# Kernel tuning notes

Hardware: AMD Instinct MI355X
Metric: run time of the kernel (lower is better)

## Reference

```python
import jax, jax.numpy as jnp
import numpy as np

B, T, H, L = 32, 256, 1024, 2
FORGET_BIAS = 1.0


def setup_inputs() -> dict:
    key = jax.random.key(0)
    k1, k2, k3, k4 = jax.random.split(key, 4)
    x = jax.random.normal(k1, (B, T, H), dtype=jnp.float32)
    lengths = jax.random.randint(k2, (B,), 1, T + 1, dtype=jnp.int32)
    Wx = jax.random.normal(k3, (L, H, 4 * H), dtype=jnp.float32) * 0.02
    Wh = jax.random.normal(k4, (L, H, 4 * H), dtype=jnp.float32) * 0.02
    b = jnp.zeros((L, 4 * H), dtype=jnp.float32)
    return {"x": x, "lengths": lengths, "Wx": Wx, "Wh": Wh, "b": b}


def _lstm_layer(x, lengths, Wx, Wh, b):
    """One TF-style LSTM layer over time with dynamic_rnn length masking.
    Gate order (i, j, f, o), forget_bias added to f. Returns (outputs, (h_T, c_T))."""
    Bb, Tt, _ = x.shape
    Hh = Wh.shape[0]
    # precompute input projections for all steps: [B, T, 4H]
    xproj = jnp.einsum('bti,ig->btg', x, Wx) + b

    def step(carry, inp):
        h, c = carry
        xt, t = inp  # xt: [B, 4H], t: scalar step index
        z = xt + h @ Wh  # [B, 4H]
        i, j, f, o = jnp.split(z, 4, axis=-1)
        c_new = jax.nn.sigmoid(f + FORGET_BIAS) * c + jax.nn.sigmoid(i) * jnp.tanh(j)
        h_new = jax.nn.sigmoid(o) * jnp.tanh(c_new)
        mask = (t < lengths)[:, None]  # [B,1]
        h2 = jnp.where(mask, h_new, h)
        c2 = jnp.where(mask, c_new, c)
        out = jnp.where(mask, h_new, 0.0)  # dynamic_rnn zeros outputs past length
        return (h2, c2), out

    init = (jnp.zeros((Bb, Hh), x.dtype), jnp.zeros((Bb, Hh), x.dtype))
    (hT, cT), outs = jax.lax.scan(step, init, (xproj.transpose(1, 0, 2), jnp.arange(Tt)))
    return outs.transpose(1, 0, 2), (hT, cT)


def reference(x, lengths, Wx, Wh, b):
    inp = x
    hs, cs = [], []
    for l in range(L):  # fixed small layer stack
        inp, (hT, cT) = _lstm_layer(inp, lengths, Wx[l], Wh[l], b[l])
        hs.append(hT)
        cs.append(cT)
    # rnnout: [B,T,H]; hidden: per-layer final (c,h) like TF LSTMStateTuple
    return inp, jnp.stack(cs), jnp.stack(hs)
```

## Files before the change

### kernel.cpp

```cpp
#include <hip/hip_runtime.h>

typedef unsigned short u16;
typedef unsigned int u32;
typedef unsigned long long u64;
typedef __attribute__((ext_vector_type(8))) short short8;
typedef __attribute__((ext_vector_type(4))) float f32x4;
typedef __attribute__((ext_vector_type(4))) u32 u32x4;
typedef __attribute__((ext_vector_type(2))) u32 u32x2;

#define RN_ 8388608
#define MFMA16(a, b, c) __builtin_amdgcn_mfma_f32_16x16x32_bf16(a, b, c, 0, 0, 0)

__device__ __forceinline__ u16 f2bf(float f) {
  union { float f; u32 u; } v; v.f = f;
  u32 r = v.u + 0x7fffu + ((v.u >> 16) & 1u);
  return (u16)(r >> 16);
}
__device__ __forceinline__ float bf2f(u16 h) {
  union { u32 u; float f; } v; v.u = ((u32)h) << 16;
  return v.f;
}
__device__ __forceinline__ u32 pk2(float a, float b) {
  return (u32)f2bf(a) | ((u32)f2bf(b) << 16);
}
__device__ __forceinline__ int permcol(int R) {
  return (R & 3) * 1024 + ((R >> 5) << 3) + ((R >> 2) & 7);
}
__device__ __forceinline__ float sigm(float x) { return 1.f / (1.f + __expf(-x)); }
__device__ __forceinline__ float tanh_(float x) {
  float e = __expf(2.f * x);
  return 1.f - 2.f / (e + 1.f);
}

__global__ __launch_bounds__(256) void transpose_convert(
    const float* __restrict__ Wx, const float* __restrict__ Wh,
    u16* __restrict__ WxT1, u16* __restrict__ WxT2,
    u16* __restrict__ WhT1, u16* __restrict__ WhT2) {
  __shared__ float lds[64][65];
  const int bid = blockIdx.x, tid = threadIdx.x;
  const int sel = bid >> 10;
  const int tile = bid & 1023;
  const int kt = tile & 15, rt = tile >> 4;
  const float* src;
  u16* dst;
  if (sel == 0)      { src = Wx;                       dst = WxT1; }
  else if (sel == 1) { src = Wx + (size_t)1024 * 4096; dst = WxT2; }
  else if (sel == 2) { src = Wh;                       dst = WhT1; }
  else               { src = Wh + (size_t)1024 * 4096; dst = WhT2; }
#pragma unroll
  for (int ii = 0; ii < 16; ++ii) {
    int idx = ii * 256 + tid;
    int r = idx >> 6, c = idx & 63;
    int run = c >> 3, u = c & 7;
    int blkLoc = run >> 2, gate = run & 3;
    int g = gate * 1024 + (rt * 2 + blkLoc) * 8 + u;
    lds[r][blkLoc * 32 + u * 4 + gate] = src[(size_t)(kt * 64 + r) * 4096 + g];
  }
  __syncthreads();
#pragma unroll
  for (int ii = 0; ii < 16; ++ii) {
    int idx = ii * 256 + tid;
    int rw = idx >> 6, cw = idx & 63;
    dst[(size_t)(rt * 64 + rw) * 1024 + kt * 64 + cw] = f2bf(lds[cw][rw]);
  }
}

template <int IS2>
__device__ void gemm_grp(char* smem, int gb,
    const float* __restrict__ Af32, const u16* __restrict__ Ahp,
    const u16* __restrict__ Bt, const float* __restrict__ bias,
    u16* __restrict__ Cring, const int* flags, int* gdone) {
  u16* As = (u16*)smem;
  u16* Bs = (u16*)(smem + 16384);
  const int tid = threadIdx.x;
  const int lane = tid & 63, w = tid >> 6;
  const int wm = w >> 1, wn = w & 1;
  const int l15 = lane & 15, lq = lane >> 4;
  const int srow = tid >> 2, qd = tid & 3;
  const u32 rsw = (u32)((l15 & 7) << 4);

  for (int c = 0; c < 16; ++c) {
    if (w == 0) {
      const int thrA = IS2 ? 16 * (c + 1) : 16 * c - 48;
      const int thrB = 16 * c - 48;
      while (1) {
        bool ok = true;
        if (lane < 16) {
          u32x4 fv;
          const u32x4* fp = (const u32x4*)flags + lane;
          asm volatile("global_load_dwordx4 %0, %1, off sc0 sc1"
                       : "=v"(fv) : "v"(fp) : "memory");
          asm volatile("s_waitcnt vmcnt(0)" ::: "memory");
          ok = (int)fv[0] >= thrA && (int)fv[1] >= thrA &&
               (int)fv[2] >= thrA && (int)fv[3] >= thrA;
        } else if (IS2 && lane < 32) {
          u32x4 fv;
          const u32x4* fp = (const u32x4*)(flags + 64) + (lane - 16);
          asm volatile("global_load_dwordx4 %0, %1, off sc0 sc1"
                       : "=v"(fv) : "v"(fp) : "memory");
          asm volatile("s_waitcnt vmcnt(0)" ::: "memory");
          ok = (int)fv[0] >= thrB && (int)fv[1] >= thrB &&
               (int)fv[2] >= thrB && (int)fv[3] >= thrB;
        }
        if (__all(ok)) break;
        __builtin_amdgcn_s_sleep(8);
      }
    }
    __syncthreads();

    for (int e = 0; e < 2; ++e) {
      const int ti = gb * 2 + e;
      const int mg = ti >> 5, ng = ti & 31;

      f32x4 acc[4][4];
#pragma unroll
      for (int i = 0; i < 4; ++i)
#pragma unroll
        for (int j = 0; j < 4; ++j) acc[i][j] = (f32x4){0.f, 0.f, 0.f, 0.f};

      for (int kt = 0; kt < 16; ++kt) {
        u32x4 aw[2][2], bv[2][2];
#pragma unroll
        for (int rr = 0; rr < 2; ++rr) {
          int row = rr * 64 + srow;
          const u32x4* bp = (const u32x4*)(Bt + (size_t)(ng * 128 + row) * 1024 + kt * 64 + qd * 16);
          bv[rr][0] = bp[0]; bv[rr][1] = bp[1];
          int rg = 512 * c + mg * 128 + row;
          if (IS2) {
            int tq = rg >> 5, b2 = rg & 31;
            int p = kt * 8 + qd * 2;
            const char* ap = (const char*)Ahp + (size_t)tq * 65536 +
                             (size_t)(p * 32 + b2) * 16;
            asm volatile("global_load_dwordx4 %0, %1, off sc0 sc1"
                         : "=v"(aw[rr][0]) : "v"(ap) : "memory");
            asm volatile("global_load_dwordx4 %0, %1, off sc0 sc1"
                         : "=v"(aw[rr][1]) : "v"(ap + 512) : "memory");
          } else {
            const f32x4* ap = (const f32x4*)(Af32 +
                ((size_t)(rg & 31) * 256 + (rg >> 5)) * 1024 + kt * 64 + qd * 16);
            f32x4 a0 = ap[0], a1 = ap[1], a2 = ap[2], a3 = ap[3];
            aw[rr][0][0] = pk2(a0[0], a0[1]); aw[rr][0][1] = pk2(a0[2], a0[3]);
            aw[rr][0][2] = pk2(a1[0], a1[1]); aw[rr][0][3] = pk2(a1[2], a1[3]);
            aw[rr][1][0] = pk2(a2[0], a2[1]); aw[rr][1][1] = pk2(a2[2], a2[3]);
            aw[rr][1][2] = pk2(a3[0], a3[1]); aw[rr][1][3] = pk2(a3[2], a3[3]);
          }
        }
        __syncthreads();
        if (IS2) {
          asm volatile("s_waitcnt vmcnt(0)" ::: "memory");
          __builtin_amdgcn_sched_barrier(0);
        }
#pragma unroll
        for (int rr = 0; rr < 2; ++rr) {
          int row = rr * 64 + srow;
          u32 sw = (u32)((row & 7) << 4);
          int base = row * 128 + qd * 32;
          *(u32x4*)((char*)As + ((base) ^ sw)) = aw[rr][0];
          *(u32x4*)((char*)As + ((base + 16) ^ sw)) = aw[rr][1];
          *(u32x4*)((char*)Bs + ((base) ^ sw)) = bv[rr][0];
          *(u32x4*)((char*)Bs + ((base + 16) ^ sw)) = bv[rr][1];
        }
        __syncthreads();
#pragma unroll
        for (int k2 = 0; k2 < 2; ++k2) {
          short8 af[4], bf[4];
#pragma unroll
          for (int f = 0; f < 4; ++f) {
            af[f] = *(const short8*)((const char*)As +
                     (((wm * 64 + f * 16 + l15) * 128 + k2 * 64 + lq * 16) ^ rsw));
            bf[f] = *(const short8*)((const char*)Bs +
                     (((wn * 64 + f * 16 + l15) * 128 + k2 * 64 + lq * 16) ^ rsw));
          }
#pragma unroll
          for (int fi = 0; fi < 4; ++fi)
#pragma unroll
            for (int fj = 0; fj < 4; ++fj)
              acc[fi][fj] = MFMA16(af[fi], bf[fj], acc[fi][fj]);
        }
      }
#pragma unroll
      for (int fj = 0; fj < 4; ++fj) {
        int gc = ng * 128 + wn * 64 + fj * 16 + l15;
        float bvv = bias[permcol(gc)];
#pragma unroll
        for (int fi = 0; fi < 4; ++fi) {
          int rr0 = (c & 3) * 512 + mg * 128 + wm * 64 + fi * 16 + lq * 4;
#pragma unroll
          for (int r = 0; r < 4; ++r) {
            u32 vv = (u32)f2bf(acc[fi][fj][r] + bvv);
            const u16* cp = Cring + (size_t)(rr0 + r) * 4096 + gc;
            asm volatile("global_store_short %0, %1, off sc0 sc1"
                         :: "v"(cp), "v"(vv) : "memory");
          }
        }
      }
      __syncthreads();
    }
    asm volatile("s_waitcnt vmcnt(0)" ::: "memory");
    if (tid == 0)
      __hip_atomic_fetch_add(gdone + c, 1, __ATOMIC_RELAXED, __HIP_MEMORY_SCOPE_AGENT);
  }
}

template <int L>
__device__ void scan_grp(char* smem, int nb,
    const u16* __restrict__ xpring, const u16* __restrict__ Wt,
    const int* __restrict__ lengths, u64* hpub,
    int* flags_self, const int* gdone,
    float* __restrict__ outp, float* __restrict__ csf, float* __restrict__ hsf) {
  f32x4* partv = (f32x4*)smem;
  u16* h_stage = (u16*)(smem + 32768);
  float* out_stage = (float*)(smem + 33792);
  const int tid = threadIdx.x;
  const int lane = tid & 63, w = tid >> 6;
  const int l15 = lane & 15, q = lane >> 4;
  const int b = (w & 1) * 16 + l15;
  const int u0 = (w >> 1) * 4 + q;
  const int len = lengths[b];

  short8 afr[4][8];
#pragma unroll
  for (int tt = 0; tt < 4; ++tt)
#pragma unroll
    for (int ks = 0; ks < 8; ++ks)
      afr[tt][ks] = *(const short8*)(Wt + (size_t)(nb * 64 + tt * 16 + l15) * 1024 +
                                     w * 256 + ks * 32 + q * 8);

  f32x4 acc[4][2];
#pragma unroll
  for (int tt = 0; tt < 4; ++tt)
#pragma unroll
    for (int bc = 0; bc < 2; ++bc) acc[tt][bc] = (f32x4){0.f, 0.f, 0.f, 0.f};
  float c0 = 0.f, h0 = 0.f, c1 = 0.f, h1 = 0.f;

  for (int t = 0; t < 256; ++t) {
    if (w == 0) {
      const int cidx = t >> 4;
      while (1) {
        bool ok = true;
        if (lane < 16) {
          u32x4 fv;
          const u32x4* fp = (const u32x4*)flags_self + lane;
          asm volatile("global_load_dwordx4 %0, %1, off sc0 sc1"
                       : "=v"(fv) : "v"(fp) : "memory");
          asm volatile("s_waitcnt vmcnt(0)" ::: "memory");
          ok = (int)fv[0] >= t && (int)fv[1] >= t && (int)fv[2] >= t && (int)fv[3] >= t;
        } else if (lane == 16) {
          u32 cd;
          const int* gp = gdone + cidx;
          asm volatile("global_load_dword %0, %1, off sc0 sc1"
                       : "=v"(cd) : "v"(gp) : "memory");
          asm volatile("s_waitcnt vmcnt(0)" ::: "memory");
          ok = (int)cd >= 64;
        }
        if (__all(ok)) break;
        __builtin_amdgcn_s_sleep(1);
      }
    }
    __syncthreads();

    const u16* xa = xpring + ((size_t)((t >> 4) & 3) * 512 + (t & 15) * 32 + b) * 4096 +
                    nb * 64 + u0 * 4;
    u32x2 xpv0, xpv1;
    asm volatile("global_load_dwordx2 %0, %1, off sc0 sc1"
                 : "=v"(xpv0) : "v"(xa) : "memory");
    asm volatile("global_load_dwordx2 %0, %1, off sc0 sc1"
                 : "=v"(xpv1) : "v"(xa + 32) : "memory");

    if (t > 0) {
      const char* hp = (const char*)hpub + (size_t)(t - 1) * 65536;
      short8 bfv[16];
#pragma unroll
      for (int i = 0; i < 16; ++i) {
        const int ks = i >> 1, bc = i & 1;
        const char* p = hp + (((w * 32 + ks * 4 + q) * 32 + bc * 16 + l15) << 4);
        asm volatile("global_load_dwordx4 %0, %1, off sc0 sc1"
                     : "=v"(bfv[i]) : "v"(p) : "memory");
      }
      asm volatile("s_waitcnt vmcnt(0)" ::: "memory");
      __builtin_amdgcn_sched_barrier(0);
#pragma unroll
      for (int i = 0; i < 16; ++i) {
        const int ks = i >> 1, bc = i & 1;
        acc[0][bc] = MFMA16(afr[0][ks], bfv[i], acc[0][bc]);
        acc[1][bc] = MFMA16(afr[1][ks], bfv[i], acc[1][bc]);
        acc[2][bc] = MFMA16(afr[2][ks], bfv[i], acc[2][bc]);
        acc[3][bc] = MFMA16(afr[3][ks], bfv[i], acc[3][bc]);
      }
    } else {
      asm volatile("s_waitcnt vmcnt(0)" ::: "memory");
      __builtin_amdgcn_sched_barrier(0);
    }

#pragma unroll
    for (int tt = 0; tt < 4; ++tt)
#pragma unroll
      for (int bc = 0; bc < 2; ++bc) {
        partv[(w * 8 + tt * 2 + bc) * 64 + lane] = acc[tt][bc];
        acc[tt][bc] = (f32x4){0.f, 0.f, 0.f, 0.f};
      }
    __syncthreads();
    f32x4 s0 = (f32x4){0.f, 0.f, 0.f, 0.f};
    f32x4 s1 = (f32x4){0.f, 0.f, 0.f, 0.f};
#pragma unroll
    for (int w2 = 0; w2 < 4; ++w2) {
      s0 += partv[(w2 * 8 + w) * 64 + lane];
      s1 += partv[(w2 * 8 + 4 + w) * 64 + lane];
    }

    bool mk = t < len;
    {
      float zi = s0[0] + bf2f((u16)(xpv0[0] & 0xffffu));
      float zj = s0[1] + bf2f((u16)(xpv0[0] >> 16));
      float zf = s0[2] + bf2f((u16)(xpv0[1] & 0xffffu)) + 1.f;
      float zo = s0[3] + bf2f((u16)(xpv0[1] >> 16));
      float cn = sigm(zf) * c0 + sigm(zi) * tanh_(zj);
      float hn = sigm(zo) * tanh_(cn);
      c0 = mk ? cn : c0;
      h0 = mk ? hn : h0;
      float ov = mk ? hn : 0.f;
      h_stage[b * 16 + u0] = f2bf(ov);
      if (L) out_stage[b * 16 + u0] = ov;
    }
    {
      float zi = s1[0] + bf2f((u16)(xpv1[0] & 0xffffu));
      float zj = s1[1] + bf2f((u16)(xpv1[0] >> 16));
      float zf = s1[2] + bf2f((u16)(xpv1[1] & 0xffffu)) + 1.f;
      float zo = s1[3] + bf2f((u16)(xpv1[1] >> 16));
      float cn = sigm(zf) * c1 + sigm(zi) * tanh_(zj);
      float hn = sigm(zo) * tanh_(cn);
      c1 = mk ? cn : c1;
      h1 = mk ? hn : h1;
      float ov = mk ? hn : 0.f;
      h_stage[b * 16 + u0 + 8] = f2bf(ov);
      if (L) out_stage[b * 16 + u0 + 8] = ov;
    }
    __syncthreads();

    if (tid < 64) {
      int p = tid >> 5, bb = tid & 31;
      const u64* hsrc = (const u64*)h_stage;
      u64 v0 = hsrc[bb * 4 + p * 2], v1 = hsrc[bb * 4 + p * 2 + 1];
      u64* hd = hpub + (size_t)t * 8192 + ((size_t)((nb * 2 + p) * 32 + bb)) * 2;
      __hip_atomic_store(hd, v0, __ATOMIC_RELAXED, __HIP_MEMORY_SCOPE_AGENT);
      __hip_atomic_store(hd + 1, v1, __ATOMIC_RELAXED, __HIP_MEMORY_SCOPE_AGENT);
    }
    asm volatile("s_waitcnt vmcnt(0)" ::: "memory");
    if (tid == 0)
      __hip_atomic_store(flags_self + nb, t + 1, __ATOMIC_RELAXED,
                         __HIP_MEMORY_SCOPE_AGENT);
    if (L && tid < 128) {
      int bb = tid >> 2, part = tid & 3;
      f32x4 ov = *(const f32x4*)(out_stage + bb * 16 + part * 4);
      *(f32x4*)(outp + ((size_t)bb * 256 + t) * 1024 + nb * 16 + part * 4) = ov;
    }
  }
  csf[L * 32768 + b * 1024 + nb * 16 + u0] = c0;
  csf[L * 32768 + b * 1024 + nb * 16 + u0 + 8] = c1;
  hsf[L * 32768 + b * 1024 + nb * 16 + u0] = h0;
  hsf[L * 32768 + b * 1024 + nb * 16 + u0 + 8] = h1;
}

__global__ __launch_bounds__(256, 1) void lstm_pipe(
    const float* __restrict__ x, const int* __restrict__ lengths,
    const float* __restrict__ bias,
    const u16* __restrict__ WxT1, const u16* __restrict__ WxT2,
    const u16* __restrict__ WhT1, const u16* __restrict__ WhT2,
    u16* xp1ring, u16* xp2ring,
    u64* hpub1, u64* hpub2, int* flags, float* outp) {
  __shared__ __align__(16) char smem[35840];
  int* g1done = flags + 128;
  int* g2done = flags + 144;
  const int bid = blockIdx.x;
  float* csf = outp + RN_;
  float* hsf = csf + 65536;
  if (bid < 64)
    gemm_grp<0>(smem, bid, x, nullptr, WxT1, bias, xp1ring, flags, g1done);
  else if (bid < 128)
    scan_grp<0>(smem, bid - 64, xp1ring, WhT1, lengths, hpub1, flags, g1done,
                outp, csf, hsf);
  else if (bid < 192)
    gemm_grp<1>(smem, bid - 128, nullptr, (const u16*)hpub1, WxT2, bias + 4096,
                xp2ring, flags, g2done);
  else
    scan_grp<1>(smem, bid - 192, xp2ring, WhT2, lengths, hpub2, flags + 64, g2done,
                outp, csf, hsf);
}

#define WS_WXT1 0u
#define WS_WXT2 (8u << 20)
#define WS_WHT1 (16u << 20)
#define WS_WHT2 (24u << 20)
#define WS_XP1 (32u << 20)
#define WS_XP2 (48u << 20)
#define WS_HPUB1 (64u << 20)
#define WS_HPUB2 (80u << 20)
#define WS_FLAGS (96u << 20)

extern "C" void kernel_launch(void* const* d_in, const int* in_sizes, int n_in,
                              void* d_out, int out_size, void* d_ws, size_t ws_size,
                              hipStream_t stream) {
  const float* x = (const float*)d_in[0];
  const int* lengths = (const int*)d_in[1];
  const float* Wx = (const float*)d_in[2];
  const float* Wh = (const float*)d_in[3];
  const float* bias = (const float*)d_in[4];
  float* outp = (float*)d_out;

  if (ws_size < (size_t)WS_FLAGS + 4096) return;

  char* ws = (char*)d_ws;
  u16* WxT1 = (u16*)(ws + WS_WXT1);
  u16* WxT2 = (u16*)(ws + WS_WXT2);
  u16* WhT1 = (u16*)(ws + WS_WHT1);
  u16* WhT2 = (u16*)(ws + WS_WHT2);
  u16* xp1ring = (u16*)(ws + WS_XP1);
  u16* xp2ring = (u16*)(ws + WS_XP2);
  u64* hpub1 = (u64*)(ws + WS_HPUB1);
  u64* hpub2 = (u64*)(ws + WS_HPUB2);
  int* flags = (int*)(ws + WS_FLAGS);

  hipMemsetAsync(flags, 0, 2048, stream);
  transpose_convert<<<4096, 256, 0, stream>>>(Wx, Wh, WxT1, WxT2, WhT1, WhT2);
  lstm_pipe<<<256, 256, 0, stream>>>(x, lengths, bias, WxT1, WxT2, WhT1, WhT2,
                                     xp1ring, xp2ring, hpub1, hpub2, flags, outp);
}
```

Baseline: 1.269 ms.

## Replace per-step flag barrier with sentinel-polled hidden-state data in recurrent loop

The per-timestep flag poll and block barrier in the recurrent LSTM loop is replaced by polling the published hidden-state data itself. The buffer is pre-filled with 0xFF sentinels, and a step is ready once no loaded word equals all-ones. Per-block flags are now published only every 16 steps, and h is stored as a single dwordx4 instead of two 64-bit atomics. This removes a global handshake and barrier from the serial critical path, but adds a 32 MB memset per call. It also relies on real bf16 pairs never forming 0xFFFFFFFF and on 16-byte stores landing atomically.

```diff
diff --git a/kernel.cpp b/kernel.cpp
--- a/kernel.cpp
+++ b/kernel.cpp
@@ -91,6 +91,7 @@
           asm volatile("global_load_dwordx4 %0, %1, off sc0 sc1"
                        : "=v"(fv) : "v"(fp) : "memory");
           asm volatile("s_waitcnt vmcnt(0)" ::: "memory");
+          __builtin_amdgcn_sched_barrier(0);
           ok = (int)fv[0] >= thrA && (int)fv[1] >= thrA &&
                (int)fv[2] >= thrA && (int)fv[3] >= thrA;
         } else if (IS2 && lane < 32) {
@@ -99,6 +100,7 @@
           asm volatile("global_load_dwordx4 %0, %1, off sc0 sc1"
                        : "=v"(fv) : "v"(fp) : "memory");
           asm volatile("s_waitcnt vmcnt(0)" ::: "memory");
+          __builtin_amdgcn_sched_barrier(0);
           ok = (int)fv[0] >= thrB && (int)fv[1] >= thrB &&
                (int)fv[2] >= thrB && (int)fv[3] >= thrB;
         }
@@ -234,30 +236,25 @@
   float c0 = 0.f, h0 = 0.f, c1 = 0.f, h1 = 0.f;
 
   for (int t = 0; t < 256; ++t) {
-    if (w == 0) {
-      const int cidx = t >> 4;
-      while (1) {
-        bool ok = true;
-        if (lane < 16) {
-          u32x4 fv;
-          const u32x4* fp = (const u32x4*)flags_self + lane;
-          asm volatile("global_load_dwordx4 %0, %1, off sc0 sc1"
-                       : "=v"(fv) : "v"(fp) : "memory");
-          asm volatile("s_waitcnt vmcnt(0)" ::: "memory");
-          ok = (int)fv[0] >= t && (int)fv[1] >= t && (int)fv[2] >= t && (int)fv[3] >= t;
-        } else if (lane == 16) {
-          u32 cd;
-          const int* gp = gdone + cidx;
-          asm volatile("global_load_dword %0, %1, off sc0 sc1"
-                       : "=v"(cd) : "v"(gp) : "memory");
-          asm volatile("s_waitcnt vmcnt(0)" ::: "memory");
-          ok = (int)cd >= 64;
-        }
-        if (__all(ok)) break;
-        __builtin_amdgcn_s_sleep(1);
-      }
-    }
-    __syncthreads();
+    if ((t & 15) == 0) {
+      if (w == 0) {
+        const int cidx = t >> 4;
+        while (1) {
+          bool ok = true;
+          if (lane == 0) {
+            u32 cd;
+            asm volatile("global_load_dword %0, %1, off sc0 sc1"
+                         : "=v"(cd) : "v"(gdone + cidx) : "memory");
+            asm volatile("s_waitcnt vmcnt(0)" ::: "memory");
+            __builtin_amdgcn_sched_barrier(0);
+            ok = (int)cd >= 64;
+          }
+          if (__all(ok)) break;
+          __builtin_amdgcn_s_sleep(2);
+        }
+      }
+      __syncthreads();
+    }
 
     const u16* xa = xpring + ((size_t)((t >> 4) & 3) * 512 + (t & 15) * 32 + b) * 4096 +
                     nb * 64 + u0 * 4;
@@ -270,14 +267,26 @@
     if (t > 0) {
       const char* hp = (const char*)hpub + (size_t)(t - 1) * 65536;
       short8 bfv[16];
-#pragma unroll
-      for (int i = 0; i < 16; ++i) {
-        const int ks = i >> 1, bc = i & 1;
-        const char* p = hp + (((w * 32 + ks * 4 + q) * 32 + bc * 16 + l15) << 4);
-        asm volatile("global_load_dwordx4 %0, %1, off sc0 sc1"
-                     : "=v"(bfv[i]) : "v"(p) : "memory");
-      }
-      asm volatile("s_waitcnt vmcnt(0)" ::: "memory");
+      while (1) {
+#pragma unroll
+        for (int i = 0; i < 16; ++i) {
+          const int ks = i >> 1, bc = i & 1;
+          const char* p = hp + (((w * 32 + ks * 4 + q) * 32 + bc * 16 + l15) << 4);
+          asm volatile("global_load_dwordx4 %0, %1, off sc0 sc1"
+                       : "=v"(bfv[i]) : "v"(p) : "memory");
+        }
+        asm volatile("s_waitcnt vmcnt(0)" ::: "memory");
+        __builtin_amdgcn_sched_barrier(0);
+        bool ok = true;
+#pragma unroll
+        for (int i = 0; i < 16; ++i) {
+          u32x4 vv = __builtin_bit_cast(u32x4, bfv[i]);
+          ok = ok && (vv[0] != 0xFFFFFFFFu) && (vv[1] != 0xFFFFFFFFu) &&
+               (vv[2] != 0xFFFFFFFFu) && (vv[3] != 0xFFFFFFFFu);
+        }
+        if (__all(ok)) break;
+        __builtin_amdgcn_s_sleep(1);
+      }
       __builtin_amdgcn_sched_barrier(0);
 #pragma unroll
       for (int i = 0; i < 16; ++i) {
@@ -339,16 +348,18 @@
 
     if (tid < 64) {
       int p = tid >> 5, bb = tid & 31;
-      const u64* hsrc = (const u64*)h_stage;
-      u64 v0 = hsrc[bb * 4 + p * 2], v1 = hsrc[bb * 4 + p * 2 + 1];
-      u64* hd = hpub + (size_t)t * 8192 + ((size_t)((nb * 2 + p) * 32 + bb)) * 2;
-      __hip_atomic_store(hd, v0, __ATOMIC_RELAXED, __HIP_MEMORY_SCOPE_AGENT);
-      __hip_atomic_store(hd + 1, v1, __ATOMIC_RELAXED, __HIP_MEMORY_SCOPE_AGENT);
-    }
-    asm volatile("s_waitcnt vmcnt(0)" ::: "memory");
-    if (tid == 0)
-      __hip_atomic_store(flags_self + nb, t + 1, __ATOMIC_RELAXED,
-                         __HIP_MEMORY_SCOPE_AGENT);
+      u32x4 pv = *(const u32x4*)((const char*)h_stage + bb * 32 + p * 16);
+      char* hd = (char*)hpub + (size_t)t * 65536 +
+                 (size_t)((nb * 2 + p) * 32 + bb) * 16;
+      asm volatile("global_store_dwordx4 %0, %1, off sc0 sc1"
+                   :: "v"(hd), "v"(pv) : "memory");
+    }
+    if (((t + 1) & 15) == 0 && w == 0) {
+      asm volatile("s_waitcnt vmcnt(0)" ::: "memory");
+      if (tid == 0)
+        __hip_atomic_store(flags_self + nb, t + 1, __ATOMIC_RELAXED,
+                           __HIP_MEMORY_SCOPE_AGENT);
+    }
     if (L && tid < 128) {
       int bb = tid >> 2, part = tid & 3;
       f32x4 ov = *(const f32x4*)(out_stage + bb * 16 + part * 4);
@@ -421,6 +432,7 @@
   int* flags = (int*)(ws + WS_FLAGS);
 
   hipMemsetAsync(flags, 0, 2048, stream);
+  hipMemsetAsync(hpub1, 0xFF, 32u << 20, stream);
   transpose_convert<<<4096, 256, 0, stream>>>(Wx, Wh, WxT1, WxT2, WhT1, WhT2);
   lstm_pipe<<<256, 256, 0, stream>>>(x, lengths, bias, WxT1, WxT2, WhT1, WhT2,
                                      xp1ring, xp2ring, hpub1, hpub2, flags, outp);
```

Result: faster. 1.232 ms (-2.9%).
